# Kernel tuning notes

Hardware: AMD Instinct MI355X
Metric: run time of the kernel (lower is better)

The kernel has to match this reference:

```python
import math
import jax, jax.numpy as jnp
import numpy as np

EPS = 1e-4
FMAX = 18  # max filtersize for scale clamped to 2.5: ceil(3*2^2.5+0.5)=18 -> kernel 37x37
KSZ = 2 * FMAX + 1


def _conv2d(x, w, b):
    # 3x3 conv, padding 1, NCHW / OIHW (cross-correlation, matches torch)
    y = jax.lax.conv_general_dilated(x, w, (1, 1), [(1, 1), (1, 1)],
                                     dimension_numbers=('NCHW', 'OIHW', 'NCHW'))
    return y + b[None, :, None, None]


def _basis_filters(scale):
    # scale: [B] -> [B,3,K,K] (g, dgdx, dgdy), masked to the per-sample support
    std = 2.0 ** scale                              # [B]
    fs = jnp.ceil(3.0 * std + 0.5)                  # per-sample filtersize
    x = jnp.arange(-FMAX, FMAX + 1, dtype=jnp.float32)          # [K]
    m = (jnp.abs(x)[None, :] <= fs[:, None]).astype(jnp.float32)  # [B,K] support mask
    e = jnp.exp(-0.5 * (x[None, :] / std[:, None]) ** 2) * m      # masked 1D gaussian [B,K]
    g = e[:, :, None] * e[:, None, :]                              # [B,K,K]
    g = g / jnp.sum(g, axis=(1, 2), keepdims=True)
    c = (-x[None, :] / (std[:, None] ** 3 * 2.0 * math.pi)) * e    # [B,K]
    dgdx = c[:, :, None] * e[:, None, :]   # varies along first spatial dim (x[0])
    dgdx = dgdx / jnp.sum(jnp.abs(dgdx), axis=(1, 2), keepdims=True)
    dgdy = e[:, :, None] * c[:, None, :]   # varies along second spatial dim (x[1])
    dgdy = dgdy / jnp.sum(jnp.abs(dgdy), axis=(1, 2), keepdims=True)
    return jnp.stack([g, dgdx, dgdy], axis=1)  # [B,3,K,K]


def setup_inputs() -> dict:
    key = jax.random.key(0)
    ks = jax.random.split(key, 7)
    B, H, W = 8, 512, 512
    batch = jax.random.uniform(ks[0], (B, 3, H, W), dtype=jnp.float32)
    gcm = jnp.array([[0.06, 0.63, 0.27], [0.3, 0.04, -0.35], [0.34, -0.6, 0.17]],
                    dtype=jnp.float32)
    w1 = jax.random.normal(ks[1], (16, 3, 3, 3), dtype=jnp.float32) * 0.1
    b1 = jax.random.normal(ks[2], (16,), dtype=jnp.float32) * 0.01
    w2 = jax.random.normal(ks[3], (16, 16, 3, 3), dtype=jnp.float32) * 0.1
    b2 = jax.random.normal(ks[4], (16,), dtype=jnp.float32) * 0.01
    w3 = jax.random.normal(ks[5], (1, 16, 3, 3), dtype=jnp.float32) * 0.1
    b3 = jax.random.normal(ks[6], (1,), dtype=jnp.float32) * 0.01
    return {"batch": batch, "gcm": gcm, "w1": w1, "b1": b1,
            "w2": w2, "b2": b2, "w3": w3, "b3": b3}


def reference(batch, gcm, w1, b1, w2, b2, w3, b3):
    B, _, H, W = batch.shape
    # ---- RGB order prior (non-differentiable, no_grad in torch) ----
    oh = lambda i: jax.nn.one_hot(i, 3, axis=1, dtype=batch.dtype)
    mx = jnp.argmax(batch, axis=1)                 # first max
    mn = jnp.argmin(batch, axis=1)
    bf = batch[:, ::-1]
    mx2 = 2 - jnp.argmax(bf, axis=1)               # last max
    mn2 = 2 - jnp.argmin(bf, axis=1)
    RGB_order = jax.lax.stop_gradient(
        0.5 * (oh(mx) + oh(mx2)) - 0.5 * (oh(mn) + oh(mn2)))  # [B,3,H,W]

    # ---- per-sample adaptive scale from small CNN ----
    h = jax.nn.silu(_conv2d(batch, w1, b1))
    h = jax.nn.silu(_conv2d(h, w2, b2))
    s = _conv2d(h, w3, b3)
    scale = jnp.clip(jnp.mean(s, axis=(1, 2, 3)), -2.5, 2.5)   # [B]

    # ---- Gaussian color model ----
    xg = jnp.einsum('ij,bjhw->bihw', gcm, batch)  # [B,3,H,W] -> (E, El, Ell)

    # ---- per-sample Gaussian basis convolution, batched via grouped conv ----
    basis = _basis_filters(scale)                                  # [B,3,K,K]
    xin = xg.reshape(1, B * 3, H, W)
    wk = jnp.broadcast_to(basis[:, None], (B, 3, 3, KSZ, KSZ)).reshape(B * 9, 1, KSZ, KSZ)
    out = jax.lax.conv_general_dilated(xin, wk, (1, 1), [(FMAX, FMAX), (FMAX, FMAX)],
                                       feature_group_count=B * 3,
                                       dimension_numbers=('NCHW', 'OIHW', 'NCHW'))
    out = out.reshape(B, 3, 3, H, W)   # [B, chan(E/El/Ell), filt(g/dx/dy), H, W]
    E = out[:, 0, 0:1]
    Ex = out[:, 0, 1:2]
    Ey = out[:, 0, 2:3]
    El = out[:, 1, 0:1]
    Ell = out[:, 2, 0:1]

    Hf = jnp.arctan(El / (Ell + EPS))
    S = jnp.log((El ** 2 + Ell ** 2) / (E ** 2 + EPS) + EPS)
    Ww = jnp.arctan((Ex / (E + EPS)) ** 2 + (Ey / (E + EPS)) ** 2)
    return jnp.concatenate([Hf, S, RGB_order, Ww], axis=1)  # [B,6,H,W]
```

## Files before the change

### kernel.cpp

```cpp
#include <hip/hip_runtime.h>
#include <hip/hip_bf16.h>

constexpr int BN = 8, HH = 512, WW = 512;
constexpr int PIX = HH * WW;
constexpr float EPSF = 1e-4f;

__device__ __forceinline__ float b2f(__hip_bfloat16 x) { return __bfloat162float(x); }
__device__ __forceinline__ __hip_bfloat16 f2b(float x) { return __float2bfloat16(x); }
__device__ __forceinline__ unsigned short bfbits(float x) {
    union { __hip_bfloat16 b; unsigned short u; } cv; cv.b = f2b(x); return cv.u;
}
__device__ __forceinline__ float ubf(unsigned short u) {
    union { unsigned int i; float f; } c; c.i = ((unsigned int)u) << 16; return c.f;
}
__device__ __forceinline__ unsigned int cvtpk(float lo, float hi) {
    unsigned int r;
    asm("v_cvt_pk_bf16_f32 %0, %1, %2" : "=v"(r) : "v"(lo), "v"(hi));
    return r;
}
__device__ __forceinline__ float silu(float a) {
    return a * __builtin_amdgcn_rcpf(1.f + __expf(-a));
}

typedef __attribute__((ext_vector_type(8))) short bf16x8;
typedef __attribute__((ext_vector_type(4))) float f32x4;

#define MF(acc, A, B) (acc) = __builtin_amdgcn_mfma_f32_16x16x32_bf16((A), (B), (acc), 0, 0, 0)

__device__ __forceinline__ bf16x8 ldb(const unsigned short* s, int off16) {
    const uint2* p = (const uint2*)(s + off16);
    uint2 a = p[0], c = p[1];
    union { uint4 u; bf16x8 v; } cv;
    cv.u = make_uint4(a.x, a.y, c.x, c.y);
    return cv.v;
}

constexpr int OFF_TOT = 0;
constexpr int OFF_ROW0 = 128;
constexpr int OFF_ROW1 = 256;
constexpr int OFF_COL0 = 384;
constexpr int OFF_COL1 = 512;
constexpr int OFF_COR = 640;
constexpr int OFF_W1R = 1280;
constexpr int OFF_WR  = 2048;
constexpr int OFF_AFR = 8192;
constexpr size_t OFF_TP0 = 262144;
constexpr size_t SZ_TPH = (size_t)BN * PIX * 2;
constexpr size_t SZ_TPF = (size_t)BN * PIX * 4;
constexpr size_t OFF_TP1 = OFF_TP0 + SZ_TPH;
constexpr size_t OFF_TP2 = OFF_TP1 + SZ_TPF;
constexpr size_t OFF_TP3 = OFF_TP2 + SZ_TPF;
constexpr size_t WS_NEEDED = OFF_TP3 + SZ_TPH;

__global__ void prep_kernel(const float* __restrict__ w1, const float* __restrict__ w2,
                            float* __restrict__ wsf) {
    int t = threadIdx.x;
    for (int i = t; i < 640; i += 256) wsf[i] = 0.f;
    unsigned short* ab = (unsigned short*)(wsf + OFF_WR);
    for (int idx = t; idx < 5120; idx += 256) {
        int part = idx / 2560;
        int id = idx - part * 2560;
        int ks = id >> 9, rem = id & 511, lane = rem >> 3, j = id & 7;
        int oc = lane & 15, q = lane >> 4;
        int k = q * 8 + j;
        int tap = 2 * ks + (k >> 4), ic = k & 15;
        float val = (tap <= 8) ? w2[oc * 144 + ic * 9 + tap] : 0.f;
        float hv = b2f(f2b(val));
        ab[idx] = (part == 0) ? bfbits(val) : bfbits(val - hv);
    }
    unsigned short* a1 = (unsigned short*)(wsf + OFF_W1R);
    for (int idx = t; idx < 1024; idx += 256) {
        int part = idx >> 9;
        int id = idx & 511;
        int lane = id >> 3, j = id & 7;
        int oc = lane & 15, q = lane >> 4;
        int k = q * 8 + j;
        float val = (k < 27) ? w1[oc * 27 + k] : 0.f;
        float hv = b2f(f2b(val));
        a1[idx] = (part == 0) ? bfbits(val) : bfbits(val - hv);
    }
}

__global__ __launch_bounds__(256) void conv12_kernel(const float* __restrict__ batch,
                                                     const unsigned short* __restrict__ w1buf,
                                                     const float* __restrict__ b1,
                                                     const unsigned short* __restrict__ abuf,
                                                     const float* __restrict__ b2v,
                                                     float* __restrict__ wsf,
                                                     float* __restrict__ out) {
    __shared__ unsigned short stb[3][12][68];
    __shared__ uint4 h1s[10 * 66 * 2];
    __shared__ float part[4][16];

    int tx = threadIdx.x;
    int lane = tx & 63, wave = tx >> 6;
    int n = lane & 15, q = lane >> 4;
    int w0 = blockIdx.x * 64, h0 = blockIdx.y * 8, b = blockIdx.z;

    union { uint4 u; bf16x8 v; } cv;
    const float* pb = batch + (size_t)(b * 3) * PIX;

    unsigned int* stw = (unsigned int*)&stb[0][0][0];
    for (int i = tx; i < 1224; i += 256) {
        int ch = i / 408, rem = i - ch * 408;
        int r = rem / 34, c2 = rem - r * 34;
        int gh = h0 - 2 + r, gw = w0 - 2 + 2 * c2;
        const float* p = pb + (size_t)ch * PIX + (size_t)gh * WW;
        bool rok = (gh >= 0) && (gh < HH);
        float v0 = (rok && gw >= 0 && gw < WW) ? p[gw] : 0.f;
        float v1 = (rok && gw + 1 >= 0 && gw + 1 < WW) ? p[gw + 1] : 0.f;
        stw[i] = cvtpk(v0, v1);
    }

    bf16x8 w1h, w1l;
    const uint4* w14 = (const uint4*)w1buf;
    cv.u = w14[lane];      w1h = cv.v;
    cv.u = w14[64 + lane]; w1l = cv.v;
    int koff[8];
#pragma unroll
    for (int j = 0; j < 8; j++) {
        int k = q * 8 + j;
        int kk = (k < 27) ? k : 0;
        int ic = kk / 9, rem = kk - ic * 9, kh = rem / 3, kw = rem - kh * 3;
        koff[j] = ic * 816 + kh * 68 + kw;
    }
    float b1q[4];
#pragma unroll
    for (int r = 0; r < 4; r++) b1q[r] = b1[q * 4 + r];
    bool hiq = (q == 3);
    __syncthreads();

    const unsigned short* sptr = &stb[0][0][0];
    unsigned int* hw = (unsigned int*)h1s;
    int i_c = wave * 16 + n;
    int r_c = (unsigned)i_c / 66u; int c_c = i_c - r_c * 66;
    int base_c = r_c * 68 + c_c;
    unsigned short x0 = sptr[base_c + koff[0]], x1 = sptr[base_c + koff[1]];
    unsigned short x2 = sptr[base_c + koff[2]], x3 = sptr[base_c + koff[3]];
    unsigned short x4 = sptr[base_c + koff[4]], x5 = sptr[base_c + koff[5]];
    unsigned short x6 = sptr[base_c + koff[6]], x7 = sptr[base_c + koff[7]];
    int g = wave;
    for (int gi = 0; gi < 11; gi++) {
        unsigned short y0 = 0, y1 = 0, y2 = 0, y3 = 0, y4 = 0, y5 = 0, y6 = 0, y7 = 0;
        int i_n = 0, c_n = 0;
        if (gi < 10) {
            i_n = (g + 4) * 16 + n; if (i_n > 659) i_n = 659;
            int r_n = (unsigned)i_n / 66u; c_n = i_n - r_n * 66;
            int base_n = r_n * 68 + c_n;
            y0 = sptr[base_n + koff[0]]; y1 = sptr[base_n + koff[1]];
            y2 = sptr[base_n + koff[2]]; y3 = sptr[base_n + koff[3]];
            y4 = sptr[base_n + koff[4]]; y5 = sptr[base_n + koff[5]];
            y6 = sptr[base_n + koff[6]]; y7 = sptr[base_n + koff[7]];
        }
        union { unsigned int w[4]; bf16x8 v; } bb;
        bb.w[0] = (unsigned int)x0 | ((unsigned int)x1 << 16);
        bb.w[1] = (unsigned int)x2 | ((unsigned int)x3 << 16);
        bb.w[2] = (unsigned int)x4 | ((unsigned int)x5 << 16);
        bb.w[3] = (unsigned int)x6 | ((unsigned int)x7 << 16);
        if (hiq) {
            bb.w[1] &= 0xFFFFu; bb.w[2] = 0u; bb.w[3] = 0u;
        }
        f32x4 a = {0, 0, 0, 0};
        MF(a, w1h, bb.v);
        MF(a, w1l, bb.v);
        int rr_ = (unsigned)i_c / 66u;
        int gh = h0 - 1 + rr_, gw = w0 - 1 + c_c;
        bool ok = ((unsigned)gh < (unsigned)HH) && ((unsigned)gw < (unsigned)WW);
        unsigned int p0 = cvtpk(silu(a[0] + b1q[0]), silu(a[1] + b1q[1]));
        unsigned int p1 = cvtpk(silu(a[2] + b1q[2]), silu(a[3] + b1q[3]));
        p0 = ok ? p0 : 0u;
        p1 = ok ? p1 : 0u;
        int swz = (c_c >> 2) & 1;
        int slot = i_c * 2 + ((q >= 2) ? (swz ^ 1) : swz);
        *(uint2*)&hw[slot * 4 + (q & 1) * 2] = make_uint2(p0, p1);
        x0 = y0; x1 = y1; x2 = y2; x3 = y3; x4 = y4; x5 = y5; x6 = y6; x7 = y7;
        i_c = i_n; c_c = c_n;
        g += 4;
    }

    for (int j = tx; j < 512; j += 256) {
        int rr = j >> 6, ccx = j & 63;
        size_t p = (size_t)(h0 + rr) * WW + (w0 + ccx);
        float v0 = pb[p], v1 = pb[(size_t)PIX + p], v2 = pb[2 * (size_t)PIX + p];
        int mx  = (v0 >= v1 && v0 >= v2) ? 0 : ((v1 >= v2) ? 1 : 2);
        int mx2 = (v2 >= v1 && v2 >= v0) ? 2 : ((v1 >= v0) ? 1 : 0);
        int mn  = (v0 <= v1 && v0 <= v2) ? 0 : ((v1 <= v2) ? 1 : 2);
        int mn2 = (v2 <= v1 && v2 <= v0) ? 2 : ((v1 <= v0) ? 1 : 0);
#pragma unroll
        for (int c = 0; c < 3; c++) {
            float r = 0.5f * ((float)(c == mx) + (float)(c == mx2))
                    - 0.5f * ((float)(c == mn) + (float)(c == mn2));
            out[(size_t)(b * 6 + 2 + c) * PIX + p] = r;
        }
    }
    __syncthreads();

    bf16x8 ah[5], al[5];
    const uint4* ab4 = (const uint4*)abuf;
#pragma unroll
    for (int ks = 0; ks < 5; ks++) {
        cv.u = ab4[ks * 64 + lane];       ah[ks] = cv.v;
        cv.u = ab4[320 + ks * 64 + lane]; al[ks] = cv.v;
    }
    float b2q[4];
#pragma unroll
    for (int r = 0; r < 4; r++) b2q[r] = b2v[q * 4 + r];

    float tt[4] = {0, 0, 0, 0};
    float cs0[4] = {0, 0, 0, 0};
    float cs1[4] = {0, 0, 0, 0};
    for (int rloc = 0; rloc < 2; rloc++) {
        int row = wave * 2 + rloc;
        int grow = h0 + row;
        f32x4 acc[4] = {{0,0,0,0},{0,0,0,0},{0,0,0,0},{0,0,0,0}};
#pragma unroll
        for (int ks = 0; ks < 5; ks++) {
            int tap = 2 * ks + (q >> 1); if (tap > 8) tap = 8;
            int dh = tap / 3 - 1, dw = tap % 3 - 1;
            int half = q & 1;
            int lr = row + 1 + dh;
#pragma unroll
            for (int t = 0; t < 4; t++) {
                int c = 1 + dw + t * 16 + n;
                cv.u = h1s[(lr * 66 + c) * 2 + (half ^ ((c >> 2) & 1))];
                MF(acc[t], ah[ks], cv.v);
                MF(acc[t], al[ks], cv.v);
            }
        }
        float sv[4][4];
#pragma unroll
        for (int t = 0; t < 4; t++)
#pragma unroll
            for (int r = 0; r < 4; r++)
                sv[t][r] = silu(acc[t][r] + b2q[r]);
#pragma unroll
        for (int r = 0; r < 4; r++) tt[r] += sv[0][r] + sv[1][r] + sv[2][r] + sv[3][r];
        if (grow == 0 || grow == HH - 1) {
            int off = (grow == 0) ? OFF_ROW0 : OFF_ROW1;
#pragma unroll
            for (int r = 0; r < 4; r++) {
                float x = sv[0][r] + sv[1][r] + sv[2][r] + sv[3][r];
#pragma unroll
                for (int d = 1; d < 16; d <<= 1) x += __shfl_xor(x, d, 64);
                if (n == 0) atomicAdd(&wsf[off + b * 16 + q * 4 + r], x);
            }
        }
        if (blockIdx.x == 0 && n == 0)
#pragma unroll
            for (int r = 0; r < 4; r++) cs0[r] += sv[0][r];
        if (blockIdx.x == 7 && n == 15)
#pragma unroll
            for (int r = 0; r < 4; r++) cs1[r] += sv[3][r];
        if ((grow == 0 || grow == HH - 1)) {
            int hi = (grow == 0) ? 0 : 1;
            if (blockIdx.x == 0 && n == 0)
#pragma unroll
                for (int r = 0; r < 4; r++)
                    wsf[OFF_COR + ((b * 2 + hi) * 2 + 0) * 16 + q * 4 + r] = sv[0][r];
            if (blockIdx.x == 7 && n == 15)
#pragma unroll
                for (int r = 0; r < 4; r++)
                    wsf[OFF_COR + ((b * 2 + hi) * 2 + 1) * 16 + q * 4 + r] = sv[3][r];
        }
    }
    if (blockIdx.x == 0 && n == 0)
#pragma unroll
        for (int r = 0; r < 4; r++) atomicAdd(&wsf[OFF_COL0 + b * 16 + q * 4 + r], cs0[r]);
    if (blockIdx.x == 7 && n == 15)
#pragma unroll
        for (int r = 0; r < 4; r++) atomicAdd(&wsf[OFF_COL1 + b * 16 + q * 4 + r], cs1[r]);
#pragma unroll
    for (int r = 0; r < 4; r++) {
        float x = tt[r];
#pragma unroll
        for (int d = 1; d < 16; d <<= 1) x += __shfl_xor(x, d, 64);
        tt[r] = x;
    }
    if (n == 0)
#pragma unroll
        for (int r = 0; r < 4; r++) part[wave][q * 4 + r] = tt[r];
    __syncthreads();
    if (tx < 16)
        atomicAdd(&wsf[OFF_TOT + b * 16 + tx],
                  part[0][tx] + part[1][tx] + part[2][tx] + part[3][tx]);
}

__global__ void filter_kernel(const float* __restrict__ w3, const float* __restrict__ b3,
                              float* __restrict__ wsf) {
    int b = blockIdx.x, t = threadIdx.x;
    __shared__ float red[160];
    float val = 0.f;
    if (t < 144) {
        int ic = t / 9, tap = t % 9, kh = tap / 3, kw = tap % 3;
        float T = wsf[OFF_TOT + b * 16 + ic];
        int hi = -1, wi = -1;
        if (kh == 0) { T -= wsf[OFF_ROW1 + b * 16 + ic]; hi = 1; }
        else if (kh == 2) { T -= wsf[OFF_ROW0 + b * 16 + ic]; hi = 0; }
        if (kw == 0) { T -= wsf[OFF_COL1 + b * 16 + ic]; wi = 1; }
        else if (kw == 2) { T -= wsf[OFF_COL0 + b * 16 + ic]; wi = 0; }
        if (hi >= 0 && wi >= 0) T += wsf[OFF_COR + ((b * 2 + hi) * 2 + wi) * 16 + ic];
        val = w3[t] * T;
    }
    red[t] = val;
    __syncthreads();
    __shared__ float sh_mean;
    if (t == 0) {
        float S = 0.f;
        for (int i = 0; i < 144; i++) S += red[i];
        sh_mean = b3[0] + S * (1.f / (float)PIX);
    }
    __syncthreads();
    float scale = fminf(2.5f, fmaxf(-2.5f, sh_mean));
    float sd = exp2f(scale);
    float fs = ceilf(3.f * sd + 0.5f);
    float e = 0.f, c = 0.f;
    if (t < 37) {
        float x = (float)(t - 18);
        if (fabsf(x) <= fs) {
            float qq = x / sd;
            e = __expf(-0.5f * qq * qq);
            c = -x / (sd * sd * sd * 6.28318530717958647692f) * e;
        }
    }
    __shared__ float sa[40], sb2[40];
    if (t < 37) { sa[t] = e; sb2[t] = fabsf(c); }
    __syncthreads();
    __shared__ float Se, Sc;
    if (t == 0) {
        float a = 0.f, d = 0.f;
        for (int i = 0; i < 37; i++) { a += sa[i]; d += sb2[i]; }
        Se = a; Sc = d;
    }
    __syncthreads();
    __shared__ float sEn[37], sCn[37];
    if (t < 37) { sEn[t] = e / Se; sCn[t] = c / Sc; }
    __syncthreads();
    if (t < 64) {
        int r = t & 15, q = t >> 4;
        uint4* afr = (uint4*)(wsf + OFF_AFR) + (size_t)b * 640 + t;
#pragma unroll
        for (int ks = 0; ks < 2; ks++) {
            unsigned short eh[8], em[8], el[8], chp[8], cmp[8];
#pragma unroll
            for (int j2 = 0; j2 < 8; j2++) {
                int d = ks * 32 + q * 8 + j2 - r;
                bool ok = (d >= 0) && (d <= 36);
                float ve = ok ? sEn[ok ? d : 0] : 0.f;
                float vc = ok ? sCn[ok ? d : 0] : 0.f;
                eh[j2] = bfbits(ve);
                float r1 = ve - ubf(eh[j2]);
                em[j2] = bfbits(r1);
                el[j2] = bfbits(r1 - ubf(em[j2]));
                chp[j2] = bfbits(vc);
                cmp[j2] = bfbits(vc - ubf(chp[j2]));
            }
#define PK2(a0, a1) ((unsigned)(a0) | ((unsigned)(a1) << 16))
            afr[(ks * 3 + 0) * 64] = make_uint4(PK2(eh[0], eh[1]), PK2(eh[2], eh[3]), PK2(eh[4], eh[5]), PK2(eh[6], eh[7]));
            afr[(ks * 3 + 1) * 64] = make_uint4(PK2(em[0], em[1]), PK2(em[2], em[3]), PK2(em[4], em[5]), PK2(em[6], em[7]));
            afr[(ks * 3 + 2) * 64] = make_uint4(PK2(el[0], el[1]), PK2(el[2], el[3]), PK2(el[4], el[5]), PK2(el[6], el[7]));
            afr[(6 + ks * 2 + 0) * 64] = make_uint4(PK2(chp[0], chp[1]), PK2(chp[2], chp[3]), PK2(chp[4], chp[5]), PK2(chp[6], chp[7]));
            afr[(6 + ks * 2 + 1) * 64] = make_uint4(PK2(cmp[0], cmp[1]), PK2(cmp[2], cmp[3]), PK2(cmp[4], cmp[5]), PK2(cmp[6], cmp[7]));
#undef PK2
        }
    }
}

__global__ __launch_bounds__(256) void horiz_kernel(const float* __restrict__ batch,
                                                    const float* __restrict__ gcm,
                                                    const float* __restrict__ wsf,
                                                    unsigned short* __restrict__ tp0,
                                                    float* __restrict__ tp1,
                                                    float* __restrict__ tp2,
                                                    unsigned short* __restrict__ tp3) {
    __shared__ unsigned short sx[7 * 32 * 84];
    int tx = threadIdx.x;
    int lane = tx & 63, wave = tx >> 6;
    int n = lane & 15, q = lane >> 4;
    int j0 = blockIdx.x * 32, h0 = blockIdx.y * 32, b = blockIdx.z;
    const float* pb = batch + (size_t)(b * 3) * PIX;
    float g0 = gcm[0], g1 = gcm[1], g2 = gcm[2];
    float g3 = gcm[3], g4 = gcm[4], g5 = gcm[5];
    float g6 = gcm[6], g7 = gcm[7], g8 = gcm[8];
    float v0r[10], v1r[10], v2r[10];
#pragma unroll
    for (int it = 0; it < 10; it++) {
        int i = tx + it * 256;
        int hh = i / 80, sc = i - hh * 80;
        int gc = j0 - 18 + sc;
        float v0 = 0.f, v1 = 0.f, v2 = 0.f;
        if ((unsigned)gc < (unsigned)WW) {
            size_t p = (size_t)(h0 + hh) * WW + gc;
            v0 = pb[p]; v1 = pb[(size_t)PIX + p]; v2 = pb[2 * (size_t)PIX + p];
        }
        v0r[it] = v0; v1r[it] = v1; v2r[it] = v2;
    }
#pragma unroll
    for (int it = 0; it < 10; it++) {
        int i = tx + it * 256;
        int hh = i / 80, sc = i - hh * 80;
        float v0 = v0r[it], v1 = v1r[it], v2 = v2r[it];
        float x0 = g0 * v0 + g1 * v1 + g2 * v2;
        float x1 = g3 * v0 + g4 * v1 + g5 * v2;
        float x2 = g6 * v0 + g7 * v1 + g8 * v2;
        int o = hh * 84 + sc;
        sx[o] = bfbits(x0);
        unsigned short h1 = bfbits(x1); sx[2688 + o] = h1;
        float r1 = x1 - ubf(h1); unsigned short m1 = bfbits(r1); sx[2 * 2688 + o] = m1;
        sx[3 * 2688 + o] = bfbits(r1 - ubf(m1));
        unsigned short h2 = bfbits(x2); sx[4 * 2688 + o] = h2;
        float r2 = x2 - ubf(h2); unsigned short m2 = bfbits(r2); sx[5 * 2688 + o] = m2;
        sx[6 * 2688 + o] = bfbits(r2 - ubf(m2));
    }
    const uint4* afr = (const uint4*)(wsf + OFF_AFR) + (size_t)b * 640 + lane;
    union { uint4 u; bf16x8 v; } cv;
    bf16x8 Ae[2][3], Ac[2][2];
#pragma unroll
    for (int ks = 0; ks < 2; ks++) {
#pragma unroll
        for (int p = 0; p < 3; p++) { cv.u = afr[(ks * 3 + p) * 64]; Ae[ks][p] = cv.v; }
#pragma unroll
        for (int p = 0; p < 2; p++) { cv.u = afr[(6 + ks * 2 + p) * 64]; Ac[ks][p] = cv.v; }
    }
    __syncthreads();
    int jt = wave & 1, ht = wave >> 1;
    f32x4 a0 = {0,0,0,0}, a1 = {0,0,0,0}, a2 = {0,0,0,0}, a3 = {0,0,0,0};
    int rb = (ht * 16 + n) * 84 + jt * 16 + q * 8;
#pragma unroll
    for (int ks = 0; ks < 2; ks++) {
        int rk = rb + ks * 32;
        bf16x8 B0  = ldb(sx, rk);
        bf16x8 B1h = ldb(sx, 2688 + rk), B1m = ldb(sx, 2 * 2688 + rk), B1l = ldb(sx, 3 * 2688 + rk);
        bf16x8 B2h = ldb(sx, 4 * 2688 + rk), B2m = ldb(sx, 5 * 2688 + rk), B2l = ldb(sx, 6 * 2688 + rk);
        MF(a0, Ae[ks][0], B0); MF(a0, Ae[ks][1], B0);
        MF(a3, Ac[ks][0], B0); MF(a3, Ac[ks][1], B0);
        MF(a1, Ae[ks][0], B1h); MF(a1, Ae[ks][0], B1m); MF(a1, Ae[ks][1], B1h);
        MF(a1, Ae[ks][0], B1l); MF(a1, Ae[ks][2], B1h); MF(a1, Ae[ks][1], B1m);
        MF(a2, Ae[ks][0], B2h); MF(a2, Ae[ks][0], B2m); MF(a2, Ae[ks][1], B2h);
        MF(a2, Ae[ks][0], B2l); MF(a2, Ae[ks][2], B2h); MF(a2, Ae[ks][1], B2m);
    }
    int jo = j0 + jt * 16 + q * 4;
    int ho = h0 + ht * 16 + n;
#pragma unroll
    for (int r = 0; r < 4; r++) {
        size_t ix = ((size_t)b * 512 + (jo + r)) * 512 + ho;
        tp0[ix] = bfbits(a0[r]);
        tp1[ix] = a1[r];
        tp2[ix] = a2[r];
        tp3[ix] = bfbits(a3[r]);
    }
}

__global__ __launch_bounds__(256) void vert_kernel(const float* __restrict__ wsf,
                                                   const unsigned short* __restrict__ tp0,
                                                   const float* __restrict__ tp1,
                                                   const float* __restrict__ tp2,
                                                   const unsigned short* __restrict__ tp3,
                                                   float* __restrict__ out) {
    __shared__ unsigned short sb[8 * 32 * 84];
    int tx = threadIdx.x;
    int lane = tx & 63, wave = tx >> 6;
    int n = lane & 15, q = lane >> 4;
    int j0 = blockIdx.x * 32, r0 = blockIdx.y * 32, b = blockIdx.z;
    unsigned short w0r[10], w7r[10];
    float f1r[10], f2r[10];
#pragma unroll
    for (int it = 0; it < 10; it++) {
        int i = tx + it * 256;
        int jj = i / 80, sr = i - jj * 80;
        int gh = r0 - 18 + sr;
        unsigned short w0 = 0, w7 = 0; float f1 = 0.f, f2 = 0.f;
        if ((unsigned)gh < (unsigned)HH) {
            size_t ix = ((size_t)b * 512 + (j0 + jj)) * 512 + gh;
            w0 = tp0[ix]; f1 = tp1[ix]; f2 = tp2[ix]; w7 = tp3[ix];
        }
        w0r[it] = w0; f1r[it] = f1; f2r[it] = f2; w7r[it] = w7;
    }
#pragma unroll
    for (int it = 0; it < 10; it++) {
        int i = tx + it * 256;
        int jj = i / 80, sr = i - jj * 80;
        int o = jj * 84 + sr;
        float f1 = f1r[it], f2 = f2r[it];
        sb[o] = w0r[it];
        unsigned short h1 = bfbits(f1); sb[2688 + o] = h1;
        float r1 = f1 - ubf(h1); unsigned short m1 = bfbits(r1); sb[2 * 2688 + o] = m1;
        sb[3 * 2688 + o] = bfbits(r1 - ubf(m1));
        unsigned short h2 = bfbits(f2); sb[4 * 2688 + o] = h2;
        float r2 = f2 - ubf(h2); unsigned short m2 = bfbits(r2); sb[5 * 2688 + o] = m2;
        sb[6 * 2688 + o] = bfbits(r2 - ubf(m2));
        sb[7 * 2688 + o] = w7r[it];
    }
    const uint4* afr = (const uint4*)(wsf + OFF_AFR) + (size_t)b * 640 + lane;
    union { uint4 u; bf16x8 v; } cv;
    bf16x8 Ae[2][3], Ac[2][2];
#pragma unroll
    for (int ks = 0; ks < 2; ks++) {
#pragma unroll
        for (int p = 0; p < 3; p++) { cv.u = afr[(ks * 3 + p) * 64]; Ae[ks][p] = cv.v; }
#pragma unroll
        for (int p = 0; p < 2; p++) { cv.u = afr[(6 + ks * 2 + p) * 64]; Ac[ks][p] = cv.v; }
    }
    __syncthreads();
    int ct = wave & 1, rt = wave >> 1;
    f32x4 aE = {0,0,0,0}, aX = {0,0,0,0}, aY = {0,0,0,0}, aL = {0,0,0,0}, aLL = {0,0,0,0};
    int rb = (ct * 16 + n) * 84 + rt * 16 + q * 8;
#pragma unroll
    for (int ks = 0; ks < 2; ks++) {
        int rk = rb + ks * 32;
        bf16x8 B0  = ldb(sb, rk);
        bf16x8 B1h = ldb(sb, 2688 + rk), B1m = ldb(sb, 2 * 2688 + rk), B1l = ldb(sb, 3 * 2688 + rk);
        bf16x8 B2h = ldb(sb, 4 * 2688 + rk), B2m = ldb(sb, 5 * 2688 + rk), B2l = ldb(sb, 6 * 2688 + rk);
        bf16x8 B3  = ldb(sb, 7 * 2688 + rk);
        MF(aE, Ae[ks][0], B0); MF(aE, Ae[ks][1], B0);
        MF(aX, Ac[ks][0], B0); MF(aX, Ac[ks][1], B0);
        MF(aY, Ae[ks][0], B3); MF(aY, Ae[ks][1], B3);
        MF(aL, Ae[ks][0], B1h); MF(aL, Ae[ks][0], B1m); MF(aL, Ae[ks][1], B1h);
        MF(aL, Ae[ks][0], B1l); MF(aL, Ae[ks][2], B1h); MF(aL, Ae[ks][1], B1m);
        MF(aLL, Ae[ks][0], B2h); MF(aLL, Ae[ks][0], B2m); MF(aLL, Ae[ks][1], B2h);
        MF(aLL, Ae[ks][0], B2l); MF(aLL, Ae[ks][2], B2h); MF(aLL, Ae[ks][1], B2m);
    }
    int ho = r0 + rt * 16 + q * 4;
    int jo = j0 + ct * 16 + n;
#pragma unroll
    for (int r = 0; r < 4; r++) {
        float E = aE[r], Ex = aX[r], Ey = aY[r], El = aL[r], Ell = aLL[r];
        float Hf = atanf(El / (Ell + EPSF));
        float S = logf((El * El + Ell * Ell) / (E * E + EPSF) + EPSF);
        float rx = Ex / (E + EPSF), ry = Ey / (E + EPSF);
        float Wv = atanf(rx * rx + ry * ry);
        size_t base = (size_t)(b * 6) * PIX + (size_t)(ho + r) * WW + jo;
        out[base] = Hf;
        out[base + PIX] = S;
        out[base + 5 * (size_t)PIX] = Wv;
    }
}

extern "C" void kernel_launch(void* const* d_in, const int* in_sizes, int n_in,
                              void* d_out, int out_size, void* d_ws, size_t ws_size,
                              hipStream_t stream) {
    const float* batch = (const float*)d_in[0];
    const float* gcm   = (const float*)d_in[1];
    const float* w1    = (const float*)d_in[2];
    const float* b1    = (const float*)d_in[3];
    const float* w2    = (const float*)d_in[4];
    const float* b2    = (const float*)d_in[5];
    const float* w3    = (const float*)d_in[6];
    const float* b3    = (const float*)d_in[7];
    float* out = (float*)d_out;

    if (ws_size < WS_NEEDED) return;

    float* wsf = (float*)d_ws;
    unsigned short* tp0 = (unsigned short*)((char*)d_ws + OFF_TP0);
    float* tp1 = (float*)((char*)d_ws + OFF_TP1);
    float* tp2 = (float*)((char*)d_ws + OFF_TP2);
    unsigned short* tp3 = (unsigned short*)((char*)d_ws + OFF_TP3);

    prep_kernel<<<dim3(1), dim3(256), 0, stream>>>(w1, w2, wsf);
    conv12_kernel<<<dim3(8, 64, 8), dim3(256), 0, stream>>>(
        batch, (const unsigned short*)(wsf + OFF_W1R), b1,
        (const unsigned short*)(wsf + OFF_WR), b2, wsf, out);
    filter_kernel<<<dim3(8), dim3(160), 0, stream>>>(w3, b3, wsf);
    horiz_kernel<<<dim3(16, 16, 8), dim3(256), 0, stream>>>(batch, gcm, wsf, tp0, tp1, tp2, tp3);
    vert_kernel<<<dim3(16, 16, 8), dim3(256), 0, stream>>>(wsf, tp0, tp1, tp2, tp3, out);
}
```

Measured before the change: 224.5 us.

## Replace per-block total atomics with partial-sum buffer and simplify conv index math

Each conv block now writes its per-channel partial sums to a dedicated workspace slot, and the filter kernel reduces them, instead of issuing atomicAdds to one shared total. This removes atomic contention on 16 addresses across 512 blocks per sample. The first-conv gather loop now advances row, column and base incrementally instead of dividing by 66 each iteration. The second conv loads all four B fragments before issuing the MFMAs. In exchange the filter kernel does a serial 64-element strided reduction per thread, and the workspace offset moves.

```diff
diff --git a/kernel.cpp b/kernel.cpp
--- a/kernel.cpp
+++ b/kernel.cpp
@@ -44,7 +44,8 @@
 constexpr int OFF_W1R = 1280;
 constexpr int OFF_WR  = 2048;
 constexpr int OFF_AFR = 8192;
-constexpr size_t OFF_TP0 = 262144;
+constexpr int OFF_PART = 32768;
+constexpr size_t OFF_TP0 = 393216;
 constexpr size_t SZ_TPH = (size_t)BN * PIX * 2;
 constexpr size_t SZ_TPF = (size_t)BN * PIX * 4;
 constexpr size_t OFF_TP1 = OFF_TP0 + SZ_TPH;
@@ -132,39 +133,36 @@
 
     const unsigned short* sptr = &stb[0][0][0];
     unsigned int* hw = (unsigned int*)h1s;
+    union U8 { unsigned short h[8]; unsigned int w[4]; bf16x8 v; };
     int i_c = wave * 16 + n;
     int r_c = (unsigned)i_c / 66u; int c_c = i_c - r_c * 66;
     int base_c = r_c * 68 + c_c;
-    unsigned short x0 = sptr[base_c + koff[0]], x1 = sptr[base_c + koff[1]];
-    unsigned short x2 = sptr[base_c + koff[2]], x3 = sptr[base_c + koff[3]];
-    unsigned short x4 = sptr[base_c + koff[4]], x5 = sptr[base_c + koff[5]];
-    unsigned short x6 = sptr[base_c + koff[6]], x7 = sptr[base_c + koff[7]];
-    int g = wave;
+    U8 curv;
+#pragma unroll
+    for (int j = 0; j < 8; j++) curv.h[j] = sptr[base_c + koff[j]];
     for (int gi = 0; gi < 11; gi++) {
-        unsigned short y0 = 0, y1 = 0, y2 = 0, y3 = 0, y4 = 0, y5 = 0, y6 = 0, y7 = 0;
-        int i_n = 0, c_n = 0;
+        U8 nxtv;
+        int i_n = 0, r_n = 0, c_n = 0, base_n = 0;
         if (gi < 10) {
-            i_n = (g + 4) * 16 + n; if (i_n > 659) i_n = 659;
-            int r_n = (unsigned)i_n / 66u; c_n = i_n - r_n * 66;
-            int base_n = r_n * 68 + c_n;
-            y0 = sptr[base_n + koff[0]]; y1 = sptr[base_n + koff[1]];
-            y2 = sptr[base_n + koff[2]]; y3 = sptr[base_n + koff[3]];
-            y4 = sptr[base_n + koff[4]]; y5 = sptr[base_n + koff[5]];
-            y6 = sptr[base_n + koff[6]]; y7 = sptr[base_n + koff[7]];
-        }
-        union { unsigned int w[4]; bf16x8 v; } bb;
-        bb.w[0] = (unsigned int)x0 | ((unsigned int)x1 << 16);
-        bb.w[1] = (unsigned int)x2 | ((unsigned int)x3 << 16);
-        bb.w[2] = (unsigned int)x4 | ((unsigned int)x5 << 16);
-        bb.w[3] = (unsigned int)x6 | ((unsigned int)x7 << 16);
+            i_n = i_c + 64;
+            int wrap = (c_c >= 2);
+            c_n = wrap ? (c_c - 2) : (c_c + 64);
+            r_n = r_c + wrap;
+            base_n = base_c + (wrap ? 66 : 64);
+            if (i_n > 659) { i_n = 659; r_n = 9; c_n = 65; base_n = 677; }
+#pragma unroll
+            for (int j = 0; j < 8; j++) nxtv.h[j] = sptr[base_n + koff[j]];
+        } else {
+#pragma unroll
+            for (int j = 0; j < 4; j++) nxtv.w[j] = 0u;
+        }
         if (hiq) {
-            bb.w[1] &= 0xFFFFu; bb.w[2] = 0u; bb.w[3] = 0u;
+            curv.w[1] &= 0xFFFFu; curv.w[2] = 0u; curv.w[3] = 0u;
         }
         f32x4 a = {0, 0, 0, 0};
-        MF(a, w1h, bb.v);
-        MF(a, w1l, bb.v);
-        int rr_ = (unsigned)i_c / 66u;
-        int gh = h0 - 1 + rr_, gw = w0 - 1 + c_c;
+        MF(a, w1h, curv.v);
+        MF(a, w1l, curv.v);
+        int gh = h0 - 1 + r_c, gw = w0 - 1 + c_c;
         bool ok = ((unsigned)gh < (unsigned)HH) && ((unsigned)gw < (unsigned)WW);
         unsigned int p0 = cvtpk(silu(a[0] + b1q[0]), silu(a[1] + b1q[1]));
         unsigned int p1 = cvtpk(silu(a[2] + b1q[2]), silu(a[3] + b1q[3]));
@@ -173,9 +171,8 @@
         int swz = (c_c >> 2) & 1;
         int slot = i_c * 2 + ((q >= 2) ? (swz ^ 1) : swz);
         *(uint2*)&hw[slot * 4 + (q & 1) * 2] = make_uint2(p0, p1);
-        x0 = y0; x1 = y1; x2 = y2; x3 = y3; x4 = y4; x5 = y5; x6 = y6; x7 = y7;
-        i_c = i_n; c_c = c_n;
-        g += 4;
+        curv = nxtv;
+        i_c = i_n; r_c = r_n; c_c = c_n; base_c = base_n;
     }
 
     for (int j = tx; j < 512; j += 256) {
@@ -205,6 +202,7 @@
     float b2q[4];
 #pragma unroll
     for (int r = 0; r < 4; r++) b2q[r] = b2v[q * 4 + r];
+    int halfb = q & 1;
 
     float tt[4] = {0, 0, 0, 0};
     float cs0[4] = {0, 0, 0, 0};
@@ -217,15 +215,14 @@
         for (int ks = 0; ks < 5; ks++) {
             int tap = 2 * ks + (q >> 1); if (tap > 8) tap = 8;
             int dh = tap / 3 - 1, dw = tap % 3 - 1;
-            int half = q & 1;
             int lr = row + 1 + dh;
-#pragma unroll
-            for (int t = 0; t < 4; t++) {
-                int c = 1 + dw + t * 16 + n;
-                cv.u = h1s[(lr * 66 + c) * 2 + (half ^ ((c >> 2) & 1))];
-                MF(acc[t], ah[ks], cv.v);
-                MF(acc[t], al[ks], cv.v);
-            }
+            int c0 = 1 + dw + n;
+            const uint4* pp = &h1s[(lr * 66 + c0) * 2 + (halfb ^ ((c0 >> 2) & 1))];
+            bf16x8 B[4];
+#pragma unroll
+            for (int t = 0; t < 4; t++) { cv.u = pp[t * 32]; B[t] = cv.v; }
+#pragma unroll
+            for (int t = 0; t < 4; t++) { MF(acc[t], ah[ks], B[t]); MF(acc[t], al[ks], B[t]); }
         }
         float sv[4][4];
 #pragma unroll
@@ -280,19 +277,37 @@
 #pragma unroll
         for (int r = 0; r < 4; r++) part[wave][q * 4 + r] = tt[r];
     __syncthreads();
-    if (tx < 16)
-        atomicAdd(&wsf[OFF_TOT + b * 16 + tx],
-                  part[0][tx] + part[1][tx] + part[2][tx] + part[3][tx]);
+    if (tx < 16) {
+        int blk = blockIdx.y * 8 + blockIdx.x;
+        wsf[OFF_PART + ((size_t)b * 512 + blk) * 16 + tx] =
+            part[0][tx] + part[1][tx] + part[2][tx] + part[3][tx];
+    }
 }
 
 __global__ void filter_kernel(const float* __restrict__ w3, const float* __restrict__ b3,
                               float* __restrict__ wsf) {
     int b = blockIdx.x, t = threadIdx.x;
+    __shared__ float spart[128];
+    __shared__ float stot[16];
+    if (t < 128) {
+        int ic = t & 15, ch = t >> 4;
+        const float* pp = wsf + OFF_PART + ((size_t)b * 512 + ch * 64) * 16 + ic;
+        float s = 0.f;
+        for (int k = 0; k < 64; k++) s += pp[k * 16];
+        spart[t] = s;
+    }
+    __syncthreads();
+    if (t < 16) {
+        float a = 0.f;
+        for (int c2 = 0; c2 < 8; c2++) a += spart[c2 * 16 + t];
+        stot[t] = a;
+    }
+    __syncthreads();
     __shared__ float red[160];
     float val = 0.f;
     if (t < 144) {
         int ic = t / 9, tap = t % 9, kh = tap / 3, kw = tap % 3;
-        float T = wsf[OFF_TOT + b * 16 + ic];
+        float T = stot[ic];
         int hi = -1, wi = -1;
         if (kh == 0) { T -= wsf[OFF_ROW1 + b * 16 + ic]; hi = 1; }
         else if (kh == 2) { T -= wsf[OFF_ROW0 + b * 16 + ic]; hi = 0; }
```

Result: no change. 226.5 us (+0.9%).
